# Kernel tuning notes

Hardware: AMD Instinct MI355X
Metric: run time of the kernel (lower is better)

## Reference

```python
import jax, jax.numpy as jnp
import numpy as np

N_NODES = 50000
N_EDGES = 800000
IN_F = 128
OUT_F = 128
EDGE_F = 6


def setup_inputs() -> dict:
    key = jax.random.key(0)
    k1, k2, k3, k4, k5, k6, k7 = jax.random.split(key, 7)
    nodeFeatures = jax.random.normal(k1, (N_NODES, IN_F), dtype=jnp.float32)
    edgeIndex = jax.random.randint(k2, (N_EDGES, 2), 0, N_NODES, dtype=jnp.int64)
    edgeFeatures = jax.random.normal(k3, (N_EDGES, EDGE_F), dtype=jnp.float32)
    # nn.Linear params (kaiming-uniform-ish init scale)
    lim_n = 1.0 / np.sqrt(IN_F)
    lim_e = 1.0 / np.sqrt(EDGE_F)
    W = jax.random.uniform(k4, (IN_F, OUT_F), minval=-lim_n, maxval=lim_n, dtype=jnp.float32)
    b = jax.random.uniform(k5, (OUT_F,), minval=-lim_n, maxval=lim_n, dtype=jnp.float32)
    We = jax.random.uniform(k6, (EDGE_F, OUT_F), minval=-lim_e, maxval=lim_e, dtype=jnp.float32)
    be = jax.random.uniform(k7, (OUT_F,), minval=-lim_e, maxval=lim_e, dtype=jnp.float32)
    return {"nodeFeatures": nodeFeatures, "edgeIndex": edgeIndex,
            "edgeFeatures": edgeFeatures, "W": W, "b": b, "We": We, "be": be}


def reference(nodeFeatures, edgeIndex, edgeFeatures, W, b, We, be):
    # node linear: [N, out]
    transformed = nodeFeatures @ W + b
    # edge linear: [E, out]
    edgeMsg = edgeFeatures @ We + be
    src = edgeIndex[:, 0]
    dst = edgeIndex[:, 1]
    # per-edge message = transformed[src] + edgeMsg, scatter-add into dst
    messages = transformed[src] + edgeMsg  # [E, out]
    aggregated = jax.ops.segment_sum(messages, dst, num_segments=nodeFeatures.shape[0])
    return jax.nn.relu(aggregated)
```

## Files before the change

### kernel.cpp

```cpp
#include <hip/hip_runtime.h>
#include <hip/hip_bf16.h>
#include <stdint.h>

#define IN_F 128
#define EDGE_F 6
#define TILE_E 4096
#define NBIN_PAD 256
#define PADMAX 1792

using bf16x8 = __attribute__((ext_vector_type(8))) short;
using f32x4  = __attribute__((ext_vector_type(4))) float;

__device__ __forceinline__ float bf2f(unsigned short u) {
    return __uint_as_float(((unsigned int)u) << 16);
}
__device__ __forceinline__ unsigned short f2bfbits(float f) {
    __hip_bfloat16 h = __float2bfloat16(f);
    return *reinterpret_cast<unsigned short*>(&h);
}
__device__ __forceinline__ unsigned int packbf(float a, float b) {
    return ((unsigned int)f2bfbits(b) << 16) | (unsigned int)f2bfbits(a);
}

__global__ __launch_bounds__(256) void pack_hist_cast(
        const int* __restrict__ eidx, const float* __restrict__ ef,
        uint4* __restrict__ efp, unsigned short* __restrict__ pmat,
        int n_edges, int nblk_e, int n_cast, int eb, int n_nodes,
        const float* __restrict__ nf, unsigned short* __restrict__ nfb,
        const float* __restrict__ W, const float* __restrict__ b,
        const float* __restrict__ We, const float* __restrict__ be,
        unsigned short* __restrict__ Wpack, float* __restrict__ W2pack) {
    const int tid = threadIdx.x;
    const int blk = blockIdx.x;
    __shared__ int hist[NBIN_PAD];

    if (blk == eb) {
        for (int idx = tid; idx < 16384; idx += 256) {
            int j = idx & 7, lane = (idx >> 3) & 63, ft = (idx >> 9) & 7, kb = idx >> 12;
            int k = kb * 32 + (lane >> 4) * 8 + j;
            int f = ft * 16 + (lane & 15);
            Wpack[idx] = f2bfbits(W[k * 128 + f]);
        }
        for (int idx = tid; idx < 1024; idx += 256) {
            int j = idx >> 7, f = idx & 127;
            float w = 0.f;
            if (j < 6)       w = We[j * 128 + f];
            else if (j == 6) w = b[f] + be[f];
            W2pack[idx] = w;
        }
        if (tid < 16) {
            uint4 z; z.x = z.y = z.z = z.w = 0u;
            reinterpret_cast<uint4*>(nfb + (size_t)n_nodes * IN_F)[tid] = z;
        }
    } else {
        const bool hb = (blk < nblk_e);
        if (hb) {
            hist[tid] = 0;
            __syncthreads();
        }
        const int t = blk * 256 + tid;
        if (t < n_edges) {
            const int2 pr = reinterpret_cast<const int2*>(eidx)[t];
            const float2* efs = reinterpret_cast<const float2*>(ef + (size_t)t * EDGE_F);
            const float2 f0 = efs[0], f1 = efs[1], f2 = efs[2];
            uint4 q;
            q.x = (unsigned int)pr.x | ((unsigned int)pr.y << 16);
            q.y = packbf(f0.x, f0.y);
            q.z = packbf(f1.x, f1.y);
            q.w = packbf(f2.x, f2.y);
            efp[t] = q;
        }
        if (hb) {
            const int e0 = blk * TILE_E;
#pragma unroll
            for (int i = 0; i < TILE_E / 256; ++i) {
                const int e = e0 + i * 256 + tid;
                if (e < n_edges) {
                    const int dst = reinterpret_cast<const int2*>(eidx)[e].y;
                    atomicAdd(&hist[dst >> 8], 1);
                }
            }
            __syncthreads();
            pmat[(size_t)blk * NBIN_PAD + tid] = (unsigned short)hist[tid];
        }
    }
    const int t = blk * 256 + tid;
    const int stride = gridDim.x * 256;
    for (int i = t; i < n_cast; i += stride) {
        const float4 lo = reinterpret_cast<const float4*>(nf)[2 * i];
        const float4 hi = reinterpret_cast<const float4*>(nf)[2 * i + 1];
        uint4 o;
        o.x = packbf(lo.x, lo.y); o.y = packbf(lo.z, lo.w);
        o.z = packbf(hi.x, hi.y); o.w = packbf(hi.z, hi.w);
        reinterpret_cast<uint4*>(nfb)[i] = o;
    }
}

__global__ __launch_bounds__(256) void coarse_scatter(
        const uint4* __restrict__ efp, const unsigned short* __restrict__ pmat,
        uint4* __restrict__ rec_c, int* __restrict__ gbase,
        int n_edges, int nblk_e, int nbin) {
    const int tid = threadIdx.x;
    const int blk = blockIdx.x;
    __shared__ int cur[NBIN_PAD];
    __shared__ int sc[NBIN_PAD];
    int tot = 0, pre = 0;
#pragma unroll 4
    for (int bb = 0; bb < nblk_e; ++bb) {
        const int v = pmat[(size_t)bb * NBIN_PAD + tid];
        tot += v;
        pre += (bb < blk) ? v : 0;
    }
    sc[tid] = tot;
    __syncthreads();
    for (int off = 1; off < 256; off <<= 1) {
        int t2 = (tid >= off) ? sc[tid - off] : 0;
        __syncthreads();
        sc[tid] += t2;
        __syncthreads();
    }
    const int excl = sc[tid] - tot;
    cur[tid] = excl + pre;
    if (blk == 0 && tid <= nbin) gbase[tid] = excl;
    __syncthreads();
    const int e0 = blk * TILE_E;
#pragma unroll
    for (int i = 0; i < TILE_E / 256; ++i) {
        const int e = e0 + i * 256 + tid;
        if (e < n_edges) {
            const uint4 q = efp[e];
            const int cb = q.x >> 24;
            const int pos = atomicAdd(&cur[cb], 1);
            rec_c[pos] = q;
        }
    }
}

__global__ __launch_bounds__(256) void fine_rank(
        const uint4* __restrict__ rec_c, const int* __restrict__ gbase,
        uint4* __restrict__ rec, int2* __restrict__ pr2, int n_nodes) {
    const int tid = threadIdx.x;
    const int c = blockIdx.x;
    const int rbase = gbase[c], rend = gbase[c + 1];
    const int pbase = rbase + c * PADMAX;
    __shared__ int fcnt[256];
    __shared__ int fpos[256];
    fcnt[tid] = 0;
    __syncthreads();
    for (int i = rbase + tid; i < rend; i += 256) {
        const unsigned int qx = reinterpret_cast<const unsigned int*>(rec_c)[(size_t)i * 4];
        atomicAdd(&fcnt[(qx >> 16) & 255], 1);
    }
    __syncthreads();
    const int own = fcnt[tid];
    const int ownp = (own + 7) & ~7;
    fcnt[tid] = ownp;
    __syncthreads();
    for (int off = 1; off < 256; off <<= 1) {
        int t2 = (tid >= off) ? fcnt[tid - off] : 0;
        __syncthreads();
        fcnt[tid] += t2;
        __syncthreads();
    }
    const int pexcl = fcnt[tid] - ownp;
    fpos[tid] = pexcl;
    const int n = c * 256 + tid;
    if (n < n_nodes) {
        int2 pr; pr.x = pbase + pexcl; pr.y = own;
        pr2[n] = pr;
    }
    __syncthreads();
    for (int i = rbase + tid; i < rend; i += 256) {
        const uint4 q = rec_c[i];
        const int r = atomicAdd(&fpos[(q.x >> 16) & 255], 1);
        rec[pbase + r] = q;
    }
    uint4 dmy; dmy.x = (unsigned int)n_nodes; dmy.y = dmy.z = dmy.w = 0u;
    for (int j = own; j < ownp; ++j)
        rec[pbase + pexcl + j] = dmy;
}

__global__ __launch_bounds__(256) void aggregate_bf16(
        const unsigned short* __restrict__ nfb, const uint4* __restrict__ rec,
        const int2* __restrict__ pr2, unsigned short* __restrict__ S,
        unsigned short* __restrict__ E8, int n_nodes) {
    const int lane = threadIdx.x & 63;
    const int wv = __builtin_amdgcn_readfirstlane(threadIdx.x >> 6);
    const int n = blockIdx.x * 4 + wv;
    if (n >= n_nodes) return;
    const int2 pr = pr2[n];
    const int deg = pr.y;
    const int nb = (deg + 7) >> 3;
    float ax = 0.f, ay = 0.f;
    float e0 = 0.f, e1 = 0.f, e2 = 0.f, e3 = 0.f, e4 = 0.f, e5 = 0.f;
    int i = pr.x;
    for (int bb = 0; bb < nb; ++bb, i += 8) {
        uint4 q[8];
        unsigned int u[8];
#pragma unroll
        for (int j = 0; j < 8; ++j) q[j] = rec[i + j];
#pragma unroll
        for (int j = 0; j < 8; ++j)
            u[j] = reinterpret_cast<const unsigned int*>(
                nfb + (size_t)(q[j].x & 0xFFFFu) * IN_F)[lane];
#pragma unroll
        for (int j = 0; j < 8; ++j) {
            ax += bf2f((unsigned short)u[j]);
            ay += bf2f((unsigned short)(u[j] >> 16));
            e0 += bf2f((unsigned short)q[j].y);
            e1 += bf2f((unsigned short)(q[j].y >> 16));
            e2 += bf2f((unsigned short)q[j].z);
            e3 += bf2f((unsigned short)(q[j].z >> 16));
            e4 += bf2f((unsigned short)q[j].w);
            e5 += bf2f((unsigned short)(q[j].w >> 16));
        }
    }
    unsigned short* row = S + (size_t)n * IN_F;
    reinterpret_cast<unsigned int*>(row)[lane] = packbf(ax, ay);
    if (lane == 0) {
        uint4 q;
        q.x = packbf(e0, e1);
        q.y = packbf(e2, e3);
        q.z = packbf(e4, e5);
        q.w = packbf((float)deg, 0.f);
        *reinterpret_cast<uint4*>(E8 + (size_t)n * 8) = q;
    }
}

__global__ __launch_bounds__(256) void gemm_mfma(
        const unsigned short* __restrict__ S, const unsigned short* __restrict__ E8,
        const unsigned short* __restrict__ Wpack, const float* __restrict__ W2pack,
        float* __restrict__ out, int n_nodes) {
    __shared__ __align__(16) short Wl[16384];
    __shared__ float W2l[1024];
    const int tid = threadIdx.x;
    for (int i = tid; i < 2048; i += 256)
        reinterpret_cast<uint4*>(Wl)[i] = reinterpret_cast<const uint4*>(Wpack)[i];
    for (int i = tid; i < 1024; i += 256) W2l[i] = W2pack[i];

    const int wv = tid >> 6, lane = tid & 63;
    const int m = lane & 15, quad = lane >> 4;
    const int n0 = blockIdx.x * 64 + wv * 16;

    const int arow = min(n0 + m, n_nodes - 1);
    const unsigned short* ap = S + (size_t)arow * IN_F + quad * 8;
    bf16x8 a[4];
#pragma unroll
    for (int kb = 0; kb < 4; ++kb)
        a[kb] = *reinterpret_cast<const bf16x8*>(ap + kb * 32);

    __syncthreads();

    f32x4 acc[8];
#pragma unroll
    for (int ft = 0; ft < 8; ++ft) acc[ft] = (f32x4){0.f, 0.f, 0.f, 0.f};

#pragma unroll
    for (int kb = 0; kb < 4; ++kb) {
#pragma unroll
        for (int ft = 0; ft < 8; ++ft) {
            const bf16x8 bfrag =
                reinterpret_cast<const bf16x8*>(Wl)[(kb * 8 + ft) * 64 + lane];
            acc[ft] = __builtin_amdgcn_mfma_f32_16x16x32_bf16(a[kb], bfrag, acc[ft], 0, 0, 0);
        }
    }

    float e[4][7];
#pragma unroll
    for (int r = 0; r < 4; ++r) {
        const int n = min(n0 + quad * 4 + r, n_nodes - 1);
        const uint4 q = *reinterpret_cast<const uint4*>(E8 + (size_t)n * 8);
        e[r][0] = bf2f((unsigned short)q.x); e[r][1] = bf2f((unsigned short)(q.x >> 16));
        e[r][2] = bf2f((unsigned short)q.y); e[r][3] = bf2f((unsigned short)(q.y >> 16));
        e[r][4] = bf2f((unsigned short)q.z); e[r][5] = bf2f((unsigned short)(q.z >> 16));
        e[r][6] = bf2f((unsigned short)q.w);
    }
#pragma unroll
    for (int ft = 0; ft < 8; ++ft) {
        const int f = ft * 16 + m;
        float w2[7];
#pragma unroll
        for (int j = 0; j < 7; ++j) w2[j] = W2l[j * 128 + f];
#pragma unroll
        for (int r = 0; r < 4; ++r) {
            const int n = n0 + quad * 4 + r;
            if (n < n_nodes) {
                float v = acc[ft][r];
#pragma unroll
                for (int j = 0; j < 7; ++j) v += e[r][j] * w2[j];
                out[(size_t)n * 128 + f] = fmaxf(v, 0.f);
            }
        }
    }
}

extern "C" void kernel_launch(void* const* d_in, const int* in_sizes, int n_in,
                              void* d_out, int out_size, void* d_ws, size_t ws_size,
                              hipStream_t stream) {
    const float* nf = (const float*)d_in[0];
    const int* eidx = (const int*)d_in[1];
    const float* ef = (const float*)d_in[2];
    const float* W  = (const float*)d_in[3];
    const float* b  = (const float*)d_in[4];
    const float* We = (const float*)d_in[5];
    const float* be = (const float*)d_in[6];
    float* out = (float*)d_out;

    const int n_nodes = in_sizes[0] / IN_F;
    const int n_edges = in_sizes[1] / 2;

    const int eb = (n_edges + 255) / 256;
    const int nblk_e = (n_edges + TILE_E - 1) / TILE_E;
    const int nbin = (n_nodes + 255) >> 8;
    const int n_cast = n_nodes * (IN_F / 8);

    uint4* rec   = (uint4*)d_ws;
    uint4* efp   = rec + ((size_t)n_edges + (size_t)nbin * PADMAX);
    uint4* rec_c = efp + n_edges;
    unsigned short* S = (unsigned short*)(rec_c + n_edges);
    unsigned short* E8 = S + (size_t)n_nodes * IN_F;
    unsigned short* Wpack = E8 + (size_t)n_nodes * 8;
    float* W2pack = (float*)(Wpack + 16384);
    unsigned short* pmat = (unsigned short*)(W2pack + 1024);
    int* gbase = (int*)(pmat + (size_t)nblk_e * NBIN_PAD);
    int2* pr2 = (int2*)(gbase + 260);
    unsigned short* nfb = (unsigned short*)(pr2 + n_nodes);

    pack_hist_cast<<<eb + 1, 256, 0, stream>>>(eidx, ef, efp, pmat,
                                               n_edges, nblk_e, n_cast, eb, n_nodes,
                                               nf, nfb, W, b, We, be, Wpack, W2pack);
    coarse_scatter<<<nblk_e, 256, 0, stream>>>(efp, pmat, rec_c, gbase,
                                               n_edges, nblk_e, nbin);
    fine_rank<<<nbin, 256, 0, stream>>>(rec_c, gbase, rec, pr2, n_nodes);
    aggregate_bf16<<<(n_nodes + 3) / 4, 256, 0, stream>>>(nfb, rec, pr2, S, E8, n_nodes);
    gemm_mfma<<<(n_nodes + 63) / 64, 256, 0, stream>>>(S, E8, Wpack, W2pack, out, n_nodes);
}
```

Measured before the change: 194.8 us.

## Fuse edge packing into scatter and gather two rows per wave in aggregation

Edge packing (index plus bf16 edge features) moves from the histogram kernel into the coarse scatter kernel, which removes the intermediate efp buffer and its extra write and read pass. The histogram/cast kernel now runs with a fixed grid of 2048 blocks plus a weight-packing block. The aggregation kernel has each half-wave gather a different source row with 8-byte loads, so a wave has two rows in flight at once, and the halves are combined with a cross-lane shuffle. The cost is that the scatter kernel now reads the raw fp32 features and does the bf16 conversion inside its atomic-scatter loop.

```diff
diff --git a/kernel.cpp b/kernel.cpp
--- a/kernel.cpp
+++ b/kernel.cpp
@@ -7,6 +7,7 @@
 #define TILE_E 4096
 #define NBIN_PAD 256
 #define PADMAX 1792
+#define K1_BLOCKS 2048
 
 using bf16x8 = __attribute__((ext_vector_type(8))) short;
 using f32x4  = __attribute__((ext_vector_type(4))) float;
@@ -22,10 +23,9 @@
     return ((unsigned int)f2bfbits(b) << 16) | (unsigned int)f2bfbits(a);
 }
 
-__global__ __launch_bounds__(256) void pack_hist_cast(
-        const int* __restrict__ eidx, const float* __restrict__ ef,
-        uint4* __restrict__ efp, unsigned short* __restrict__ pmat,
-        int n_edges, int nblk_e, int n_cast, int eb, int n_nodes,
+__global__ __launch_bounds__(256) void hist_cast(
+        const int* __restrict__ eidx, unsigned short* __restrict__ pmat,
+        int n_edges, int nblk_e, int n_cast, int wblk, int n_nodes,
         const float* __restrict__ nf, unsigned short* __restrict__ nfb,
         const float* __restrict__ W, const float* __restrict__ b,
         const float* __restrict__ We, const float* __restrict__ be,
@@ -34,7 +34,7 @@
     const int blk = blockIdx.x;
     __shared__ int hist[NBIN_PAD];
 
-    if (blk == eb) {
+    if (blk == wblk) {
         for (int idx = tid; idx < 16384; idx += 256) {
             int j = idx & 7, lane = (idx >> 3) & 63, ft = (idx >> 9) & 7, kb = idx >> 12;
             int k = kb * 32 + (lane >> 4) * 8 + j;
@@ -52,37 +52,20 @@
             uint4 z; z.x = z.y = z.z = z.w = 0u;
             reinterpret_cast<uint4*>(nfb + (size_t)n_nodes * IN_F)[tid] = z;
         }
-    } else {
-        const bool hb = (blk < nblk_e);
-        if (hb) {
-            hist[tid] = 0;
-            __syncthreads();
-        }
-        const int t = blk * 256 + tid;
-        if (t < n_edges) {
-            const int2 pr = reinterpret_cast<const int2*>(eidx)[t];
-            const float2* efs = reinterpret_cast<const float2*>(ef + (size_t)t * EDGE_F);
-            const float2 f0 = efs[0], f1 = efs[1], f2 = efs[2];
-            uint4 q;
-            q.x = (unsigned int)pr.x | ((unsigned int)pr.y << 16);
-            q.y = packbf(f0.x, f0.y);
-            q.z = packbf(f1.x, f1.y);
-            q.w = packbf(f2.x, f2.y);
-            efp[t] = q;
-        }
-        if (hb) {
-            const int e0 = blk * TILE_E;
-#pragma unroll
-            for (int i = 0; i < TILE_E / 256; ++i) {
-                const int e = e0 + i * 256 + tid;
-                if (e < n_edges) {
-                    const int dst = reinterpret_cast<const int2*>(eidx)[e].y;
-                    atomicAdd(&hist[dst >> 8], 1);
-                }
+    } else if (blk < nblk_e) {
+        hist[tid] = 0;
+        __syncthreads();
+        const int e0 = blk * TILE_E;
+#pragma unroll
+        for (int i = 0; i < TILE_E / 256; ++i) {
+            const int e = e0 + i * 256 + tid;
+            if (e < n_edges) {
+                const int dst = reinterpret_cast<const int2*>(eidx)[e].y;
+                atomicAdd(&hist[dst >> 8], 1);
             }
-            __syncthreads();
-            pmat[(size_t)blk * NBIN_PAD + tid] = (unsigned short)hist[tid];
-        }
+        }
+        __syncthreads();
+        pmat[(size_t)blk * NBIN_PAD + tid] = (unsigned short)hist[tid];
     }
     const int t = blk * 256 + tid;
     const int stride = gridDim.x * 256;
@@ -96,8 +79,9 @@
     }
 }
 
-__global__ __launch_bounds__(256) void coarse_scatter(
-        const uint4* __restrict__ efp, const unsigned short* __restrict__ pmat,
+__global__ __launch_bounds__(256) void pack_scatter(
+        const int* __restrict__ eidx, const float* __restrict__ ef,
+        const unsigned short* __restrict__ pmat,
         uint4* __restrict__ rec_c, int* __restrict__ gbase,
         int n_edges, int nblk_e, int nbin) {
     const int tid = threadIdx.x;
@@ -128,9 +112,15 @@
     for (int i = 0; i < TILE_E / 256; ++i) {
         const int e = e0 + i * 256 + tid;
         if (e < n_edges) {
-            const uint4 q = efp[e];
-            const int cb = q.x >> 24;
-            const int pos = atomicAdd(&cur[cb], 1);
+            const int2 pr = reinterpret_cast<const int2*>(eidx)[e];
+            const float2* efs = reinterpret_cast<const float2*>(ef + (size_t)e * EDGE_F);
+            const float2 f0 = efs[0], f1 = efs[1], f2 = efs[2];
+            uint4 q;
+            q.x = (unsigned int)pr.x | ((unsigned int)pr.y << 16);
+            q.y = packbf(f0.x, f0.y);
+            q.z = packbf(f1.x, f1.y);
+            q.w = packbf(f2.x, f2.y);
+            const int pos = atomicAdd(&cur[pr.y >> 8], 1);
             rec_c[pos] = q;
         }
     }
@@ -191,22 +181,32 @@
     const int2 pr = pr2[n];
     const int deg = pr.y;
     const int nb = (deg + 7) >> 3;
-    float ax = 0.f, ay = 0.f;
+    const int half = lane >> 5;
+    const int hl = lane & 31;
+    float a0 = 0.f, a1 = 0.f, a2 = 0.f, a3 = 0.f;
     float e0 = 0.f, e1 = 0.f, e2 = 0.f, e3 = 0.f, e4 = 0.f, e5 = 0.f;
     int i = pr.x;
     for (int bb = 0; bb < nb; ++bb, i += 8) {
         uint4 q[8];
-        unsigned int u[8];
 #pragma unroll
         for (int j = 0; j < 8; ++j) q[j] = rec[i + j];
-#pragma unroll
-        for (int j = 0; j < 8; ++j)
-            u[j] = reinterpret_cast<const unsigned int*>(
-                nfb + (size_t)(q[j].x & 0xFFFFu) * IN_F)[lane];
+        uint2 u[4];
+#pragma unroll
+        for (int p = 0; p < 4; ++p) {
+            const unsigned int sA = q[2 * p].x & 0xFFFFu;
+            const unsigned int sB = q[2 * p + 1].x & 0xFFFFu;
+            const unsigned int s = half ? sB : sA;
+            u[p] = reinterpret_cast<const uint2*>(nfb + (size_t)s * IN_F)[hl];
+        }
+#pragma unroll
+        for (int p = 0; p < 4; ++p) {
+            a0 += bf2f((unsigned short)u[p].x);
+            a1 += bf2f((unsigned short)(u[p].x >> 16));
+            a2 += bf2f((unsigned short)u[p].y);
+            a3 += bf2f((unsigned short)(u[p].y >> 16));
+        }
 #pragma unroll
         for (int j = 0; j < 8; ++j) {
-            ax += bf2f((unsigned short)u[j]);
-            ay += bf2f((unsigned short)(u[j] >> 16));
             e0 += bf2f((unsigned short)q[j].y);
             e1 += bf2f((unsigned short)(q[j].y >> 16));
             e2 += bf2f((unsigned short)q[j].z);
@@ -215,8 +215,16 @@
             e5 += bf2f((unsigned short)(q[j].w >> 16));
         }
     }
-    unsigned short* row = S + (size_t)n * IN_F;
-    reinterpret_cast<unsigned int*>(row)[lane] = packbf(ax, ay);
+    a0 += __shfl_xor(a0, 32, 64);
+    a1 += __shfl_xor(a1, 32, 64);
+    a2 += __shfl_xor(a2, 32, 64);
+    a3 += __shfl_xor(a3, 32, 64);
+    if (half == 0) {
+        uint2 o;
+        o.x = packbf(a0, a1);
+        o.y = packbf(a2, a3);
+        reinterpret_cast<uint2*>(S + (size_t)n * IN_F)[hl] = o;
+    }
     if (lane == 0) {
         uint4 q;
         q.x = packbf(e0, e1);
@@ -309,14 +317,12 @@
     const int n_nodes = in_sizes[0] / IN_F;
     const int n_edges = in_sizes[1] / 2;
 
-    const int eb = (n_edges + 255) / 256;
     const int nblk_e = (n_edges + TILE_E - 1) / TILE_E;
     const int nbin = (n_nodes + 255) >> 8;
     const int n_cast = n_nodes * (IN_F / 8);
 
     uint4* rec   = (uint4*)d_ws;
-    uint4* efp   = rec + ((size_t)n_edges + (size_t)nbin * PADMAX);
-    uint4* rec_c = efp + n_edges;
+    uint4* rec_c = rec + ((size_t)n_edges + (size_t)nbin * PADMAX);
     unsigned short* S = (unsigned short*)(rec_c + n_edges);
     unsigned short* E8 = S + (size_t)n_nodes * IN_F;
     unsigned short* Wpack = E8 + (size_t)n_nodes * 8;
@@ -326,11 +332,12 @@
     int2* pr2 = (int2*)(gbase + 260);
     unsigned short* nfb = (unsigned short*)(pr2 + n_nodes);
 
-    pack_hist_cast<<<eb + 1, 256, 0, stream>>>(eidx, ef, efp, pmat,
-                                               n_edges, nblk_e, n_cast, eb, n_nodes,
-                                               nf, nfb, W, b, We, be, Wpack, W2pack);
-    coarse_scatter<<<nblk_e, 256, 0, stream>>>(efp, pmat, rec_c, gbase,
-                                               n_edges, nblk_e, nbin);
+    hist_cast<<<K1_BLOCKS + 1, 256, 0, stream>>>(eidx, pmat,
+                                                 n_edges, nblk_e, n_cast, K1_BLOCKS,
+                                                 n_nodes, nf, nfb,
+                                                 W, b, We, be, Wpack, W2pack);
+    pack_scatter<<<nblk_e, 256, 0, stream>>>(eidx, ef, pmat, rec_c, gbase,
+                                             n_edges, nblk_e, nbin);
     fine_rank<<<nbin, 256, 0, stream>>>(rec_c, gbase, rec, pr2, n_nodes);
     aggregate_bf16<<<(n_nodes + 3) / 4, 256, 0, stream>>>(nfb, rec, pr2, S, E8, n_nodes);
     gemm_mfma<<<(n_nodes + 63) / 64, 256, 0, stream>>>(S, E8, Wpack, W2pack, out, n_nodes);
```

Result: no change. 196.8 us (+1.0%).
